# Performance work log

Hardware: AMD Instinct MI355X
Metric: run time of the kernel (lower is better)

Reference implementation:

```python
import jax, jax.numpy as jnp
import numpy as np
from jax import lax

B, T, D_IN, H, L, D_OUT = 64, 512, 256, 1024, 3, 128


def setup_inputs() -> dict:
    key = jax.random.key(0)
    ks = jax.random.split(key, 8)
    s_in = 1.0 / np.sqrt(H)  # PyTorch-style uniform-ish scale, keeps ReLU recurrence stable
    return {
        "x": jax.random.normal(ks[0], (B, T, D_IN), jnp.float32),
        "w_ih0": jax.random.normal(ks[1], (H, D_IN), jnp.float32) * s_in,
        "w_ih_rest": jax.random.normal(ks[2], (L - 1, H, H), jnp.float32) * s_in,
        "w_hh": jax.random.normal(ks[3], (L, H, H), jnp.float32) * s_in,
        "b_ih": jax.random.normal(ks[4], (L, H), jnp.float32) * s_in,
        "b_hh": jax.random.normal(ks[5], (L, H), jnp.float32) * s_in,
        "fc_w": jax.random.normal(ks[6], (D_OUT, H), jnp.float32) * s_in,
        "fc_b": jax.random.normal(ks[7], (D_OUT,), jnp.float32) * s_in,
    }


def _rnn_layer(seq, w_ih, w_hh, bi, bh):
    # seq: [B, T, d_in]; precompute input projection as one big GEMM
    pre = jnp.einsum("btd,hd->bth", seq, w_ih) + bi + bh  # [B, T, H]
    h0 = jnp.zeros((seq.shape[0], w_hh.shape[0]), seq.dtype)

    def step(h, p_t):  # h: [B, H], p_t: [B, H]
        h = jax.nn.relu(p_t + h @ w_hh.T)
        return h, h

    _, hs = lax.scan(step, h0, jnp.swapaxes(pre, 0, 1))  # [T, B, H]
    return jnp.swapaxes(hs, 0, 1)  # [B, T, H]


def reference(x, w_ih0, w_ih_rest, w_hh, b_ih, b_hh, fc_w, fc_b):
    seq = _rnn_layer(x, w_ih0, w_hh[0], b_ih[0], b_hh[0])
    for l in range(1, L):
        seq = _rnn_layer(seq, w_ih_rest[l - 1], w_hh[l], b_ih[l], b_hh[l])
    # fc on last timestep: out[:, -1, :] @ fc_w.T + fc_b
    return seq[:, -1, :] @ fc_w.T + fc_b
```

## Files before the change

kernel.cpp:

```cpp
#include <hip/hip_runtime.h>

#define NB   64
#define NT   512
#define DIN  256
#define NH   1024
#define DOUT 128

#define HS_STR 1028
#define WL_STR 20
#define RD_STR 260

typedef float f4 __attribute__((ext_vector_type(4)));
typedef float f2 __attribute__((ext_vector_type(2)));
typedef unsigned short bfr;

__device__ __forceinline__ float b2f(bfr u) {
    union { unsigned u; float f; } v; v.u = ((unsigned)u) << 16; return v.f;
}
__device__ __forceinline__ bfr f2b(float f) {
    union { float f; unsigned u; } v; v.f = f;
    unsigned r = v.u + 0x7FFFu + ((v.u >> 16) & 1u);
    return (bfr)(r >> 16);
}

template <typename T> __device__ __forceinline__ f4 load4(const T* p);
template <> __device__ __forceinline__ f4 load4<float>(const float* p) { return *(const f4*)p; }
template <> __device__ __forceinline__ f4 load4<bfr>(const bfr* p) {
    ushort4 u = *(const ushort4*)p;
    f4 r; r[0] = b2f(u.x); r[1] = b2f(u.y); r[2] = b2f(u.z); r[3] = b2f(u.w); return r;
}
template <typename T> __device__ __forceinline__ void store1(T* p, float v);
template <> __device__ __forceinline__ void store1<float>(float* p, float v) { *p = v; }
template <> __device__ __forceinline__ void store1<bfr>(bfr* p, float v) { *p = f2b(v); }
template <typename T> __device__ __forceinline__ float load1(const T* p);
template <> __device__ __forceinline__ float load1<float>(const float* p) { return *p; }
template <> __device__ __forceinline__ float load1<bfr>(const bfr* p) { return b2f(*p); }

template <int K, int LOG2CT, typename TA, typename TO>
__global__ __launch_bounds__(256)
void proj_kernel(const TA* __restrict__ A, const float* __restrict__ W,
                 const float* __restrict__ bih, const float* __restrict__ bhh,
                 TO* __restrict__ out, int tOff)
{
    __shared__ float As[16][68];
    __shared__ float Ws[16][68];
    const int tid = threadIdx.x;
    const int CTM = (1 << LOG2CT) - 1;
    const int m0 = (blockIdx.x >> 4) << 6;
    const int n0 = (blockIdx.x & 15) << 6;
    const int tm = tid & 15, tn = tid >> 4;
    const int lr = tid >> 2, lc = tid & 3;

    const int rA = m0 + lr;
    const long mrowA = (long)(rA >> LOG2CT) * NT + tOff + (rA & CTM);

    float acc[4][4] = {};
    for (int k0 = 0; k0 < K; k0 += 16) {
        f4 av = load4<TA>(&A[mrowA * K + k0 + lc * 4]);
        f4 wv = *(const f4*)&W[(n0 + lr) * K + k0 + lc * 4];
        __syncthreads();
        #pragma unroll
        for (int j = 0; j < 4; ++j) {
            As[lc * 4 + j][lr] = av[j];
            Ws[lc * 4 + j][lr] = wv[j];
        }
        __syncthreads();
        #pragma unroll
        for (int k = 0; k < 16; ++k) {
            f4 a = *(const f4*)&As[k][tm * 4];
            f4 w = *(const f4*)&Ws[k][tn * 4];
            #pragma unroll
            for (int i = 0; i < 4; ++i)
                #pragma unroll
                for (int j = 0; j < 4; ++j)
                    acc[i][j] += a[i] * w[j];
        }
    }
    #pragma unroll
    for (int j = 0; j < 4; ++j) {
        const int n = n0 + tn * 4 + j;
        const float bias = bih[n] + bhh[n];
        #pragma unroll
        for (int i = 0; i < 4; ++i)
            store1<TO>(&out[(long)(m0 + tm * 4 + i) * NH + n], acc[i][j] + bias);
    }
}

template <typename TP, int L2CT>
__global__ __launch_bounds__(256)
void copyback_kernel(const TP* __restrict__ Q, TP* __restrict__ P, int tOff)
{
    const int r = blockIdx.x, tid = threadIdx.x;
    const int b = r >> L2CT, t = r & ((1 << L2CT) - 1);
    const TP* q = Q + (long)r * NH;
    TP* p = P + ((long)b * NT + tOff + t) * NH;
    #pragma unroll
    for (int j = 0; j < 4; ++j) p[tid + j * 256] = q[tid + j * 256];
}

template <typename TP>
__global__ __launch_bounds__(512, 2)
void recur_kernel(const float* __restrict__ Whh, TP* __restrict__ P,
                  float* __restrict__ Hring, unsigned* __restrict__ sy)
{
    __shared__ float Wl[NH * WL_STR];
    __shared__ float hs[16 * HS_STR];
    float* red = hs;

    const int tid   = threadIdx.x;
    const int wg    = blockIdx.x;
    const int nBase = (wg & 63) << 4;
    const int bBase = (wg >> 6) << 4;
    const int grp   = wg >> 6;
    const int lane  = tid & 63;
    const int tb = tid & 3, tn = (tid >> 2) & 3, tk = tid >> 4;
    const int half = tid >> 8, col = (tid & 255) * 4;
    const int ob = (tid & 255) >> 4, on = tid & 15;

    #pragma unroll
    for (int r8 = 0; r8 < 8; ++r8) {
        const int r = half * 8 + r8;
        f4 w = *(const f4*)&Whh[(nBase + r) * NH + col];
        #pragma unroll
        for (int j = 0; j < 4; ++j) Wl[(col + j) * WL_STR + r] = w[j];
    }
    for (int i = tid; i < 16 * HS_STR; i += 512) hs[i] = 0.f;
    __syncthreads();

    #pragma unroll 1
    for (int ts = 0; ts < NT; ++ts) {
        float pre = 0.f; TP* pp = nullptr;
        if (tid < 256) {
            pp = &P[((long)(bBase + ob) * NT + ts) * NH + nBase + on];
            pre = load1<TP>(pp);
        }

        float acc[4][4] = {};
        #pragma unroll
        for (int kk = 0; kk < 8; ++kk) {
            const int kb = kk * 128 + tk * 4;
            f4 hv[4], wv[4];
            #pragma unroll
            for (int i = 0; i < 4; ++i)
                hv[i] = *(const f4*)&hs[(tb * 4 + i) * HS_STR + kb];
            #pragma unroll
            for (int jj = 0; jj < 4; ++jj)
                wv[jj] = *(const f4*)&Wl[(kb + jj) * WL_STR + tn * 4];
            #pragma unroll
            for (int jj = 0; jj < 4; ++jj)
                #pragma unroll
                for (int i = 0; i < 4; ++i)
                    #pragma unroll
                    for (int j = 0; j < 4; ++j)
                        acc[i][j] += hv[i][jj] * wv[jj][j];
        }
        __syncthreads();
        #pragma unroll
        for (int i = 0; i < 4; ++i) {
            f4 t; t[0] = acc[i][0]; t[1] = acc[i][1]; t[2] = acc[i][2]; t[3] = acc[i][3];
            *(f4*)&red[tk * RD_STR + (tb * 4 + i) * 16 + tn * 4] = t;
        }
        __syncthreads();

        if (tid < 256) {
            float s = 0.f;
            #pragma unroll
            for (int q = 0; q < 32; ++q) s += red[q * RD_STR + tid];
            const float h = fmaxf(s + pre, 0.f);
            store1<TP>(pp, h);
            __hip_atomic_store(&Hring[(ts & 1) * (NB * NH) + (bBase + ob) * NH + nBase + on],
                               h, __ATOMIC_RELAXED, __HIP_MEMORY_SCOPE_AGENT);
        }
        if (ts == NT - 1) break;

        __syncthreads();
        if (tid == 0)
            __hip_atomic_store(&sy[wg], (unsigned)(ts + 1),
                               __ATOMIC_RELAXED, __HIP_MEMORY_SCOPE_AGENT);

        {
            const unsigned tgt = (unsigned)(ts + 1);
            const unsigned* fp = &sy[grp * 64 + lane];
            unsigned fv = __hip_atomic_load(fp, __ATOMIC_RELAXED, __HIP_MEMORY_SCOPE_AGENT);
            while (!__all((int)(fv >= tgt))) {
                __builtin_amdgcn_s_sleep(1);
                fv = __hip_atomic_load(fp, __ATOMIC_RELAXED, __HIP_MEMORY_SCOPE_AGENT);
            }
        }

        {
            const float* hb = Hring + (ts & 1) * (NB * NH) + (long)bBase * NH + (tid << 1);
            f2 stg[16];
            #pragma unroll
            for (int r = 0; r < 16; ++r) {
                const float* a = hb + r * NH;
                asm volatile("global_load_dwordx2 %0, %1, off sc0 sc1"
                             : "=v"(stg[r]) : "v"(a) : "memory");
            }
            asm volatile("s_waitcnt vmcnt(0)" ::: "memory");
            #pragma unroll
            for (int r = 0; r < 16; ++r)
                *(f2*)&hs[r * HS_STR + (tid << 1)] = stg[r];
        }
        __syncthreads();
    }
}

template <typename TP>
__global__ __launch_bounds__(128)
void fc_kernel(const TP* __restrict__ seq, const float* __restrict__ fcw,
               const float* __restrict__ fcb, float* __restrict__ out)
{
    __shared__ float hrow[NH];
    const int b = blockIdx.x, tid = threadIdx.x;
    for (int i = tid * 4; i < NH; i += 128 * 4) {
        f4 v = load4<TP>(&seq[((long)b * NT + (NT - 1)) * NH + i]);
        *(f4*)&hrow[i] = v;
    }
    __syncthreads();
    float s = 0.f;
    const float* wr = &fcw[tid * NH];
    for (int k = 0; k < NH; k += 4) {
        f4 w = *(const f4*)&wr[k];
        s += w[0] * hrow[k] + w[1] * hrow[k + 1] + w[2] * hrow[k + 2] + w[3] * hrow[k + 3];
    }
    out[b * DOUT + tid] = s + fcb[tid];
}

template <typename TP>
static void coop_recur(const float* W, TP* P, float* Hring, unsigned* sy,
                       hipStream_t stream)
{
    hipMemsetAsync(sy, 0, 4096, stream);
    const float* Wp = W; TP* Pp = P; float* H = Hring; unsigned* s = sy;
    void* args[4] = { &Wp, &Pp, &H, &s };
    hipLaunchCooperativeKernel((const void*)recur_kernel<TP>, dim3(256), dim3(512),
                               args, 0, stream);
}

static void run_pathA(const float* x, const float* wih0, const float* wihr,
                      const float* whh, const float* bih, const float* bhh,
                      const float* fcw, const float* fcb, float* out,
                      unsigned* sy, float* Hring, float* P0, float* P1,
                      hipStream_t stream)
{
    const dim3 blk(256);
    proj_kernel<DIN, 9, float, float><<<8192, blk, 0, stream>>>(x, wih0, bih, bhh, P0, 0);
    coop_recur<float>(whh, P0, Hring, sy, stream);
    proj_kernel<NH, 9, float, float><<<8192, blk, 0, stream>>>(P0, wihr,
        bih + NH, bhh + NH, P1, 0);
    coop_recur<float>(whh + NH * NH, P1, Hring, sy, stream);
    proj_kernel<NH, 9, float, float><<<8192, blk, 0, stream>>>(P1, wihr + NH * NH,
        bih + 2 * NH, bhh + 2 * NH, P0, 0);
    coop_recur<float>(whh + 2 * (NH * NH), P0, Hring, sy, stream);
    fc_kernel<float><<<dim3(NB), dim3(128), 0, stream>>>(P0, fcw, fcb, out);
}

template <typename TP>
static void run_pathBC(const float* x, const float* wih0, const float* wihr,
                       const float* whh, const float* bih, const float* bhh,
                       const float* fcw, const float* fcb, float* out,
                       unsigned* sy, float* Hring, TP* P, TP* Q, hipStream_t stream)
{
    const dim3 blk(256);
    proj_kernel<DIN, 9, float, TP><<<8192, blk, 0, stream>>>(x, wih0, bih, bhh, P, 0);
    coop_recur<TP>(whh, P, Hring, sy, stream);
    for (int l = 1; l < 3; ++l) {
        const float* wih = wihr + (long)(l - 1) * NH * NH;
        for (int c = 0; c < NT / 32; ++c) {
            proj_kernel<NH, 5, TP, TP><<<512, blk, 0, stream>>>(P, wih, bih + l * NH,
                                                                bhh + l * NH, Q, c * 32);
            copyback_kernel<TP, 5><<<NB * 32, blk, 0, stream>>>(Q, P, c * 32);
        }
        coop_recur<TP>(whh + (long)l * NH * NH, P, Hring, sy, stream);
    }
    fc_kernel<TP><<<dim3(NB), dim3(128), 0, stream>>>(P, fcw, fcb, out);
}

extern "C" void kernel_launch(void* const* d_in, const int* in_sizes, int n_in,
                              void* d_out, int out_size, void* d_ws, size_t ws_size,
                              hipStream_t stream)
{
    (void)in_sizes; (void)n_in; (void)out_size;
    const float* x    = (const float*)d_in[0];
    const float* wih0 = (const float*)d_in[1];
    const float* wihr = (const float*)d_in[2];
    const float* whh  = (const float*)d_in[3];
    const float* bih  = (const float*)d_in[4];
    const float* bhh  = (const float*)d_in[5];
    const float* fcw  = (const float*)d_in[6];
    const float* fcb  = (const float*)d_in[7];
    float* out = (float*)d_out;

    char* ws = (char*)d_ws;
    unsigned* sy = (unsigned*)ws;
    float* Hring = (float*)(ws + 4096);
    char* base = ws + 4096 + 2ull * NB * NH * 4;

    const size_t pF32 = (size_t)NB * NT * NH * 4;
    const size_t qF32 = (size_t)NB * 32 * NH * 4;
    const size_t head = 4096 + 2ull * NB * NH * 4;
    const size_t needA = head + 2 * pF32;
    const size_t needB = head + pF32 + qF32;

    if (ws_size >= needA) {
        float* P0 = (float*)base;
        float* P1 = (float*)(base + pF32);
        run_pathA(x, wih0, wihr, whh, bih, bhh, fcw, fcb, out,
                  sy, Hring, P0, P1, stream);
    } else if (ws_size >= needB) {
        float* P = (float*)base;
        float* Q = (float*)(base + pF32);
        run_pathBC<float>(x, wih0, wihr, whh, bih, bhh, fcw, fcb, out,
                          sy, Hring, P, Q, stream);
    } else {
        bfr* P = (bfr*)base;
        bfr* Q = (bfr*)(base + pF32 / 2);
        run_pathBC<bfr>(x, wih0, wihr, whh, bih, bhh, fcw, fcb, out,
                        sy, Hring, P, Q, stream);
    }
}
```

Before: 12.29 ms.

## Keep recurrent weights in registers and split batch tile into two halves

The recurrent kernel now holds each thread's slice of W_hh in registers (64 floats per thread) instead of in a transposed LDS tile. Each workgroup processes its 16 batch rows as two halves of 8, each with its own LDS buffer, reduction and flag array, so the first half's result can be published before the second half is computed. The reduction buffer stride changes and the occupancy hint in launch_bounds is dropped. The cost is higher register pressure, an extra barrier per step, and a spin wait that polls two flag arrays.

```diff
diff --git a/kernel.cpp b/kernel.cpp
--- a/kernel.cpp
+++ b/kernel.cpp
@@ -7,8 +7,7 @@
 #define DOUT 128
 
 #define HS_STR 1028
-#define WL_STR 20
-#define RD_STR 260
+#define RD_STR 136
 
 typedef float f4 __attribute__((ext_vector_type(4)));
 typedef float f2 __attribute__((ext_vector_type(2)));
@@ -99,108 +98,158 @@
 }
 
 template <typename TP>
-__global__ __launch_bounds__(512, 2)
+__global__ __launch_bounds__(512)
 void recur_kernel(const float* __restrict__ Whh, TP* __restrict__ P,
                   float* __restrict__ Hring, unsigned* __restrict__ sy)
 {
-    __shared__ float Wl[NH * WL_STR];
-    __shared__ float hs[16 * HS_STR];
-    float* red = hs;
-
-    const int tid   = threadIdx.x;
-    const int wg    = blockIdx.x;
+    __shared__ float hsA[8 * HS_STR];
+    __shared__ float hsB[8 * HS_STR];
+    __shared__ float red[32 * RD_STR];
+
+    const int tid  = threadIdx.x;
+    const int wg   = blockIdx.x;
     const int nBase = (wg & 63) << 4;
-    const int bBase = (wg >> 6) << 4;
-    const int grp   = wg >> 6;
+    const int set   = wg >> 6;
+    const int rank  = wg & 63;
     const int lane  = tid & 63;
-    const int tb = tid & 3, tn = (tid >> 2) & 3, tk = tid >> 4;
-    const int half = tid >> 8, col = (tid & 255) * 4;
-    const int ob = (tid & 255) >> 4, on = tid & 15;
-
-    #pragma unroll
-    for (int r8 = 0; r8 < 8; ++r8) {
-        const int r = half * 8 + r8;
-        f4 w = *(const f4*)&Whh[(nBase + r) * NH + col];
+    const int tk = tid >> 4;
+    const int tn = (tid >> 1) & 7;
+    const int tb = tid & 1;
+    const int bl = tid >> 4;
+    const int nl = tid & 15;
+
+    float w0[32], w1[32];
+    {
+        const float* p0 = &Whh[(nBase + tn * 2 + 0) * NH + tk * 32];
+        const float* p1 = &Whh[(nBase + tn * 2 + 1) * NH + tk * 32];
         #pragma unroll
-        for (int j = 0; j < 4; ++j) Wl[(col + j) * WL_STR + r] = w[j];
-    }
-    for (int i = tid; i < 16 * HS_STR; i += 512) hs[i] = 0.f;
+        for (int i = 0; i < 8; ++i) {
+            *(f4*)&w0[i * 4] = *(const f4*)&p0[i * 4];
+            *(f4*)&w1[i * 4] = *(const f4*)&p1[i * 4];
+        }
+    }
+    for (int i = tid; i < 8 * HS_STR; i += 512) { hsA[i] = 0.f; hsB[i] = 0.f; }
     __syncthreads();
 
     #pragma unroll 1
     for (int ts = 0; ts < NT; ++ts) {
-        float pre = 0.f; TP* pp = nullptr;
-        if (tid < 256) {
-            pp = &P[((long)(bBase + ob) * NT + ts) * NH + nBase + on];
-            pre = load1<TP>(pp);
-        }
-
-        float acc[4][4] = {};
-        #pragma unroll
-        for (int kk = 0; kk < 8; ++kk) {
-            const int kb = kk * 128 + tk * 4;
-            f4 hv[4], wv[4];
-            #pragma unroll
-            for (int i = 0; i < 4; ++i)
-                hv[i] = *(const f4*)&hs[(tb * 4 + i) * HS_STR + kb];
-            #pragma unroll
-            for (int jj = 0; jj < 4; ++jj)
-                wv[jj] = *(const f4*)&Wl[(kb + jj) * WL_STR + tn * 4];
-            #pragma unroll
-            for (int jj = 0; jj < 4; ++jj)
+        const unsigned tgt = (unsigned)(ts + 1);
+
+        float preA = 0.f; TP* ppA = nullptr;
+        if (tid < 128) {
+            ppA = &P[((long)(set * 16 + bl) * NT + ts) * NH + nBase + nl];
+            preA = load1<TP>(ppA);
+        }
+        {
+            float acc[4][2] = {};
+            #pragma unroll
+            for (int kk = 0; kk < 8; ++kk) {
+                f4 hv[4];
                 #pragma unroll
                 for (int i = 0; i < 4; ++i)
+                    hv[i] = *(const f4*)&hsA[(tb * 4 + i) * HS_STR + tk * 32 + kk * 4];
+                #pragma unroll
+                for (int c = 0; c < 4; ++c)
                     #pragma unroll
-                    for (int j = 0; j < 4; ++j)
-                        acc[i][j] += hv[i][jj] * wv[jj][j];
-        }
-        __syncthreads();
-        #pragma unroll
-        for (int i = 0; i < 4; ++i) {
-            f4 t; t[0] = acc[i][0]; t[1] = acc[i][1]; t[2] = acc[i][2]; t[3] = acc[i][3];
-            *(f4*)&red[tk * RD_STR + (tb * 4 + i) * 16 + tn * 4] = t;
-        }
-        __syncthreads();
-
-        if (tid < 256) {
+                    for (int i = 0; i < 4; ++i) {
+                        acc[i][0] += hv[i][c] * w0[kk * 4 + c];
+                        acc[i][1] += hv[i][c] * w1[kk * 4 + c];
+                    }
+            }
+            #pragma unroll
+            for (int i = 0; i < 4; ++i) {
+                red[tk * RD_STR + (tb * 4 + i) * 16 + tn * 2 + 0] = acc[i][0];
+                red[tk * RD_STR + (tb * 4 + i) * 16 + tn * 2 + 1] = acc[i][1];
+            }
+        }
+        __syncthreads();
+        if (tid < 128) {
             float s = 0.f;
             #pragma unroll
             for (int q = 0; q < 32; ++q) s += red[q * RD_STR + tid];
-            const float h = fmaxf(s + pre, 0.f);
-            store1<TP>(pp, h);
-            __hip_atomic_store(&Hring[(ts & 1) * (NB * NH) + (bBase + ob) * NH + nBase + on],
+            const float h = fmaxf(s + preA, 0.f);
+            store1<TP>(ppA, h);
+            __hip_atomic_store(&Hring[((long)(ts & 1) << 16) + ((set * 16 + bl) << 10) + nBase + nl],
                                h, __ATOMIC_RELAXED, __HIP_MEMORY_SCOPE_AGENT);
         }
+        __syncthreads();
+        if (tid == 0 && ts < NT - 1)
+            __hip_atomic_store(&sy[(set * 2 + 0) * 64 + rank], tgt,
+                               __ATOMIC_RELAXED, __HIP_MEMORY_SCOPE_AGENT);
+
+        float preB = 0.f; TP* ppB = nullptr;
+        if (tid < 128) {
+            ppB = &P[((long)(set * 16 + 8 + bl) * NT + ts) * NH + nBase + nl];
+            preB = load1<TP>(ppB);
+        }
+        {
+            float acc[4][2] = {};
+            #pragma unroll
+            for (int kk = 0; kk < 8; ++kk) {
+                f4 hv[4];
+                #pragma unroll
+                for (int i = 0; i < 4; ++i)
+                    hv[i] = *(const f4*)&hsB[(tb * 4 + i) * HS_STR + tk * 32 + kk * 4];
+                #pragma unroll
+                for (int c = 0; c < 4; ++c)
+                    #pragma unroll
+                    for (int i = 0; i < 4; ++i) {
+                        acc[i][0] += hv[i][c] * w0[kk * 4 + c];
+                        acc[i][1] += hv[i][c] * w1[kk * 4 + c];
+                    }
+            }
+            __syncthreads();
+            #pragma unroll
+            for (int i = 0; i < 4; ++i) {
+                red[tk * RD_STR + (tb * 4 + i) * 16 + tn * 2 + 0] = acc[i][0];
+                red[tk * RD_STR + (tb * 4 + i) * 16 + tn * 2 + 1] = acc[i][1];
+            }
+        }
+        __syncthreads();
+        if (tid < 128) {
+            float s = 0.f;
+            #pragma unroll
+            for (int q = 0; q < 32; ++q) s += red[q * RD_STR + tid];
+            const float h = fmaxf(s + preB, 0.f);
+            store1<TP>(ppB, h);
+            __hip_atomic_store(&Hring[((long)(ts & 1) << 16) + ((set * 16 + 8 + bl) << 10) + nBase + nl],
+                               h, __ATOMIC_RELAXED, __HIP_MEMORY_SCOPE_AGENT);
+        }
         if (ts == NT - 1) break;
-
         __syncthreads();
         if (tid == 0)
-            __hip_atomic_store(&sy[wg], (unsigned)(ts + 1),
+            __hip_atomic_store(&sy[(set * 2 + 1) * 64 + rank], tgt,
                                __ATOMIC_RELAXED, __HIP_MEMORY_SCOPE_AGENT);
 
         {
-            const unsigned tgt = (unsigned)(ts + 1);
-            const unsigned* fp = &sy[grp * 64 + lane];
-            unsigned fv = __hip_atomic_load(fp, __ATOMIC_RELAXED, __HIP_MEMORY_SCOPE_AGENT);
-            while (!__all((int)(fv >= tgt))) {
+            const unsigned* fpA = &sy[(set * 2 + 0) * 64 + lane];
+            const unsigned* fpB = &sy[(set * 2 + 1) * 64 + lane];
+            for (;;) {
+                unsigned a = __hip_atomic_load(fpA, __ATOMIC_RELAXED, __HIP_MEMORY_SCOPE_AGENT);
+                unsigned b = __hip_atomic_load(fpB, __ATOMIC_RELAXED, __HIP_MEMORY_SCOPE_AGENT);
+                if (__all((int)(a >= tgt && b >= tgt))) break;
                 __builtin_amdgcn_s_sleep(1);
-                fv = __hip_atomic_load(fp, __ATOMIC_RELAXED, __HIP_MEMORY_SCOPE_AGENT);
             }
         }
 
         {
-            const float* hb = Hring + (ts & 1) * (NB * NH) + (long)bBase * NH + (tid << 1);
-            f2 stg[16];
-            #pragma unroll
-            for (int r = 0; r < 16; ++r) {
-                const float* a = hb + r * NH;
+            const float* hbA = Hring + ((long)(ts & 1) << 16) + ((long)(set * 16) << 10) + (tid << 1);
+            const float* hbB = hbA + (8 << 10);
+            f2 sA[8], sB[8];
+            #pragma unroll
+            for (int r = 0; r < 8; ++r)
                 asm volatile("global_load_dwordx2 %0, %1, off sc0 sc1"
-                             : "=v"(stg[r]) : "v"(a) : "memory");
-            }
+                             : "=v"(sA[r]) : "v"(hbA + (r << 10)) : "memory");
+            #pragma unroll
+            for (int r = 0; r < 8; ++r)
+                asm volatile("global_load_dwordx2 %0, %1, off sc0 sc1"
+                             : "=v"(sB[r]) : "v"(hbB + (r << 10)) : "memory");
             asm volatile("s_waitcnt vmcnt(0)" ::: "memory");
             #pragma unroll
-            for (int r = 0; r < 16; ++r)
-                *(f2*)&hs[r * HS_STR + (tid << 1)] = stg[r];
+            for (int r = 0; r < 8; ++r) {
+                *(f2*)&hsA[r * HS_STR + (tid << 1)] = sA[r];
+                *(f2*)&hsB[r * HS_STR + (tid << 1)] = sB[r];
+            }
         }
         __syncthreads();
     }
```

New measurement: 12.30 ms. No clear change (+0.1%).
